# Optimization experiments

Hardware: AMD Instinct MI355X
Metric: run time of the kernel (lower is better)

The kernel has to match this reference:

```python
import jax, jax.numpy as jnp
import numpy as np

J = 4  # number of wavelet scales


def _wavelet(P, X, mask):
    """Graph diffusion wavelet features for one (batch, time) slice.
    P: [N,N] transition matrix, X: [N,F] node features, mask: [N].
    Returns flattened pooled features [K*F], K = 1 + J + J*(J-1)/2.
    """
    P_pow = P
    F1, F2, PSI = [], [], []
    for _ in range(J):
        new_P = P_pow @ P_pow              # P^{2^{i+1}}
        psi = new_P - P_pow                # psi_i = P^{2^{i+1}} - P^{2^i}
        sc = jnp.abs(psi @ X)              # |psi_i X|  [N,F]
        F1.append(sc)
        for prev_psi in PSI:               # second order: |psi_j |psi_i X||, j < i
            F2.append(jnp.abs(prev_psi @ sc))
        PSI.append(psi)
        P_pow = new_P
    F0 = P_pow @ X                         # zeroth order: P^{2^J} X
    feats = jnp.stack([F0, *F1, *F2])      # [K, N, F]
    # pooling: mean over nodes (normalized by mask.sum()), then flatten
    return (feats.sum(axis=1) / mask.sum()).reshape(-1)


def setup_inputs() -> dict:
    key = jax.random.key(0)
    k1, k2 = jax.random.split(key)
    B, T, N, F = 8, 4, 1024, 64
    A = jax.random.uniform(k1, (B, T, N, N), dtype=jnp.float32)
    P = A / A.sum(axis=-1, keepdims=True)  # row-stochastic transition matrix
    X = jax.random.normal(k2, (B, T, N, F), dtype=jnp.float32)
    mask = jnp.ones((B, T, N), dtype=jnp.float32)
    return {"P": P, "X": X, "mask": mask}


def reference(P, X, mask):
    return jax.vmap(jax.vmap(_wavelet))(P, X, mask)  # [B, T, K*F]
```

## Files before the change

kernel.cpp:

```cpp
#include <hip/hip_runtime.h>

typedef unsigned short u16;
typedef __bf16 bfx8 __attribute__((ext_vector_type(8)));
typedef float f32x4 __attribute__((ext_vector_type(4)));
typedef unsigned short u16x4 __attribute__((ext_vector_type(4)));

#define NN 1024
#define FF 64
#define NSLICE 32
#define KFEAT 11

#define POOL_BYTES (NSLICE * KFEAT * FF * 4)
#define MSUM_OFF   POOL_BYTES
#define SLICE0     ((size_t)1 << 20)
#define MB1        (1024u * 1024u)
#define KB128      (131072u)
#define KB256      (262144u)
#define OFF_P    0u
#define OFF_PT   (2u * MB1)
#define OFF_P2   (4u * MB1)
#define OFF_XT   (6u * MB1)
#define OFF_Y2T  (6u * MB1 + 1u * KB128)
#define OFF_Y4T  (6u * MB1 + 2u * KB128)
#define OFF_Y6T  (6u * MB1 + 3u * KB128)
#define OFF_Y8T  (6u * MB1 + 4u * KB128)
#define OFF_Y10T (6u * MB1 + 5u * KB128)
#define OFF_Y12T (6u * MB1 + 6u * KB128)
#define OFF_Y14T (6u * MB1 + 7u * KB128)
#define OFF_S1T  (6u * MB1 + 8u * KB128)
#define OFF_S2T  (6u * MB1 + 9u * KB128)
#define OFF_S3T  (6u * MB1 + 10u * KB128)
#define OFF_TQ2  (6u * MB1 + 11u * KB128)
#define OFF_TQ3  (6u * MB1 + 12u * KB128)
#define OFF_TW4  (6u * MB1 + 13u * KB128)
#define OFF_TP6  (6u * MB1 + 14u * KB128)
#define OFF_Y1   (8u * MB1)
#define OFF_Y2   (8u * MB1 + 1u * KB256)
#define OFF_Y4   (8u * MB1 + 2u * KB256)
#define OFF_Y8   (8u * MB1 + 3u * KB256)
#define OFF_PS1  (8u * MB1 + 4u * KB256)
#define OFF_PS2  (8u * MB1 + 5u * KB256)
#define OFF_PS3  (8u * MB1 + 6u * KB256)
#define OFF_QS2  (8u * MB1 + 7u * KB256)
#define OFF_QS3  (8u * MB1 + 8u * KB256)
#define OFF_W4   (8u * MB1 + 9u * KB256)
#define PS_BYTES ((size_t)(11u * MB1))

#define GL16(g, l) __builtin_amdgcn_global_load_lds( \
    (const __attribute__((address_space(1))) unsigned int*)(g), \
    (__attribute__((address_space(3))) unsigned int*)(l), 16, 0, 0)


__device__ __forceinline__ u16 f2b(float v) {
  __bf16 h = (__bf16)v;
  return __builtin_bit_cast(u16, h);
}

__global__ void k_convP(const float* __restrict__ P, char* ws, int sliceBase) {
  __shared__ float tile[64][65];
  int s = blockIdx.z;
  const float* Ps = P + (size_t)(sliceBase + s) * NN * NN;
  char* base = ws + SLICE0 + (size_t)s * PS_BYTES;
  u16* Pb  = (u16*)(base + OFF_P);
  u16* PbT = (u16*)(base + OFF_PT);
  int r0 = blockIdx.y * 64, c0 = blockIdx.x * 64;
  int tid = threadIdx.x;
  int tc = tid & 15, tr = tid >> 4;
  for (int rr = 0; rr < 64; rr += 16) {
    int r = rr + tr;
    float4 v = *(const float4*)&Ps[(size_t)(r0 + r) * NN + c0 + tc * 4];
    tile[r][tc * 4 + 0] = v.x;
    tile[r][tc * 4 + 1] = v.y;
    tile[r][tc * 4 + 2] = v.z;
    tile[r][tc * 4 + 3] = v.w;
    u16x4 pk = {f2b(v.x), f2b(v.y), f2b(v.z), f2b(v.w)};
    *(u16x4*)&Pb[(size_t)(r0 + r) * NN + c0 + tc * 4] = pk;
  }
  __syncthreads();
  for (int it = 0; it < 4; ++it) {
    int oc = (tid >> 4) + it * 16;
    int ch = tid & 15;
    u16x4 pk = {f2b(tile[ch * 4 + 0][oc]), f2b(tile[ch * 4 + 1][oc]),
                f2b(tile[ch * 4 + 2][oc]), f2b(tile[ch * 4 + 3][oc])};
    *(u16x4*)&PbT[(size_t)(c0 + oc) * NN + r0 + ch * 4] = pk;
  }
}

__global__ void k_convX(const float* __restrict__ X, char* ws, int sliceBase) {
  __shared__ float tile[64][65];
  int s = blockIdx.z;
  const float* Xs = X + (size_t)(sliceBase + s) * NN * FF;
  u16* XT = (u16*)(ws + SLICE0 + (size_t)s * PS_BYTES + OFF_XT);
  int r0 = blockIdx.x * 64;
  int tx = threadIdx.x & 63, ty = threadIdx.x >> 6;
  for (int rr = 0; rr < 64; rr += 4)
    tile[rr + ty][tx] = Xs[(size_t)(r0 + rr + ty) * FF + tx];
  __syncthreads();
  for (int rr = 0; rr < 64; rr += 4)
    XT[(size_t)(rr + ty) * NN + r0 + tx] = f2b(tile[tx][rr + ty]);
}

__global__ void k_msum(const float* __restrict__ mask, float* msum) {
  int s = blockIdx.x;
  const float* m = mask + (size_t)s * NN;
  int t = threadIdx.x;
  float v = m[t] + m[t + 256] + m[t + 512] + m[t + 768];
  for (int o = 32; o; o >>= 1) v += __shfl_down(v, o);
  __shared__ float ps[4];
  if ((t & 63) == 0) ps[t >> 6] = v;
  __syncthreads();
  if (t == 0) msum[s] = ps[0] + ps[1] + ps[2] + ps[3];
}

__global__ __launch_bounds__(256)
void k_square(char* ws) {
  __shared__ u16 sh[16384];

  unsigned nwg = gridDim.x, wg = blockIdx.x;
  unsigned newid = (wg & 7) * (nwg >> 3) + (wg >> 3);
  int z = newid >> 6;
  int by = (newid >> 3) & 7, bx = newid & 7;

  char* base = ws + SLICE0 + (size_t)z * PS_BYTES;
  const u16* A  = (const u16*)(base + OFF_P);
  const u16* Bt = (const u16*)(base + OFF_PT);
  u16* C        = (u16*)(base + OFF_P2);

  const int tid = threadIdx.x;
  const int lane = tid & 63, wave = tid >> 6;
  const int wr = wave >> 1, wc = wave & 1;
  const int l16 = lane & 15, lk = lane >> 4;
  const int bm = by * 128, bn = bx * 128;

  const int pc = (((tid & 3) - (tid >> 3)) & 3) << 3;
  const u16* gA = A + (size_t)(bm + (tid >> 2)) * NN + pc;
  const u16* gB = Bt + (size_t)(bn + (tid >> 2)) * NN + pc;
  const int rot = ((lk + (l16 >> 1)) & 3) << 3;

  f32x4 acc[4][4] = {};

#define SQ_STAGE(k0, buf)                                   \
  {                                                         \
    u16* dA = sh + (buf)*4096 + wave * 512;                 \
    u16* dB = sh + 8192 + (buf)*4096 + wave * 512;          \
    GL16(gA + (k0), dA);                                    \
    GL16(gA + 64 * NN + (k0), dA + 2048);                   \
    GL16(gB + (k0), dB);                                    \
    GL16(gB + 64 * NN + (k0), dB + 2048);                   \
  }

#define SQ_COMPUTE(buf)                                                      \
  {                                                                          \
    const u16* bA = sh + (buf)*4096;                                         \
    const u16* bB = sh + 8192 + (buf)*4096;                                  \
    bfx8 af[4], bf[4];                                                       \
    _Pragma("unroll") for (int m = 0; m < 4; ++m)                            \
        af[m] = *(const bfx8*)&bA[(wr * 64 + m * 16 + l16) * 32 + rot];      \
    _Pragma("unroll") for (int n = 0; n < 4; ++n)                            \
        bf[n] = *(const bfx8*)&bB[(wc * 64 + n * 16 + l16) * 32 + rot];      \
    __builtin_amdgcn_s_setprio(1);                                           \
    _Pragma("unroll") for (int m = 0; m < 4; ++m)                            \
        _Pragma("unroll") for (int n = 0; n < 4; ++n)                        \
            acc[m][n] = __builtin_amdgcn_mfma_f32_16x16x32_bf16(             \
                af[m], bf[n], acc[m][n], 0, 0, 0);                           \
    __builtin_amdgcn_s_setprio(0);                                           \
  }

  SQ_STAGE(0, 0);
#pragma unroll 2
  for (int t = 1; t < 32; ++t) {
    SQ_STAGE(t * 32, t & 1);
    asm volatile("s_waitcnt vmcnt(4)" ::: "memory");
    __builtin_amdgcn_s_barrier();
    SQ_COMPUTE((t - 1) & 1);
    __builtin_amdgcn_s_barrier();
  }
  asm volatile("s_waitcnt vmcnt(0)" ::: "memory");
  __builtin_amdgcn_s_barrier();
  SQ_COMPUTE(1);

#pragma unroll
  for (int m = 0; m < 4; ++m) {
    int row0 = bm + wr * 64 + m * 16 + lk * 4;
#pragma unroll
    for (int n = 0; n < 4; ++n) {
      int col = bn + wc * 64 + n * 16 + l16;
#pragma unroll
      for (int r = 0; r < 4; ++r)
        C[(size_t)(row0 + r) * NN + col] = f2b(acc[m][n][r]);
    }
  }
}

struct NA {
  int a, rawK;
  int bt[3], d[3], pk[3], f[3], ta[3], tv[3];
};

__device__ __forceinline__ void nar_epilogue(
    char* base, const f32x4 (&acc)[2][2], int bm, int wr, int wc, int l16,
    int lk, int lane, int dof, int pkI, int fo, int tao, int tvo, bool doRaw,
    int rawK, int poolBase, float* __restrict__ pooled) {
  const float* D = dof >= 0 ? (const float*)(base + dof) : nullptr;
  float* F  = fo  >= 0 ? (float*)(base + fo)  : nullptr;
  u16* Ta   = tao >= 0 ? (u16*)(base + tao)   : nullptr;
  u16* Tv   = tvo >= 0 ? (u16*)(base + tvo)   : nullptr;

  float ps[2] = {0.f, 0.f};
  float pr[2] = {0.f, 0.f};

#pragma unroll
  for (int m = 0; m < 2; ++m) {
    int row0 = bm + wr * 32 + m * 16 + lk * 4;
#pragma unroll
    for (int n = 0; n < 2; ++n) {
      int col = wc * 32 + n * 16 + l16;
      float v0 = acc[m][n][0], v1 = acc[m][n][1];
      float v2 = acc[m][n][2], v3 = acc[m][n][3];
      float w0 = v0, w1 = v1, w2 = v2, w3 = v3;
      if (D) {
        w0 = v0 - D[(size_t)(row0 + 0) * FF + col];
        w1 = v1 - D[(size_t)(row0 + 1) * FF + col];
        w2 = v2 - D[(size_t)(row0 + 2) * FF + col];
        w3 = v3 - D[(size_t)(row0 + 3) * FF + col];
      }
      float a0 = fabsf(w0), a1 = fabsf(w1), a2 = fabsf(w2), a3 = fabsf(w3);
      if (pkI >= 0) ps[n] += a0 + a1 + a2 + a3;
      if (doRaw) pr[n] += v0 + v1 + v2 + v3;
      if (F) {
        F[(size_t)(row0 + 0) * FF + col] = v0;
        F[(size_t)(row0 + 1) * FF + col] = v1;
        F[(size_t)(row0 + 2) * FF + col] = v2;
        F[(size_t)(row0 + 3) * FF + col] = v3;
      }
      if (Ta) {
        u16x4 pkk = {f2b(a0), f2b(a1), f2b(a2), f2b(a3)};
        *(u16x4*)&Ta[(size_t)col * NN + row0] = pkk;
      }
      if (Tv) {
        u16x4 pkk = {f2b(v0), f2b(v1), f2b(v2), f2b(v3)};
        *(u16x4*)&Tv[(size_t)col * NN + row0] = pkk;
      }
    }
  }

  if (pkI >= 0) {
#pragma unroll
    for (int n = 0; n < 2; ++n) {
      float v = ps[n];
      v += __shfl_xor(v, 16);
      v += __shfl_xor(v, 32);
      if (lane < 16)
        atomicAdd(&pooled[poolBase + pkI * FF + wc * 32 + n * 16 + lane], v);
    }
  }
  if (doRaw) {
#pragma unroll
    for (int n = 0; n < 2; ++n) {
      float v = pr[n];
      v += __shfl_xor(v, 16);
      v += __shfl_xor(v, 32);
      if (lane < 16)
        atomicAdd(&pooled[poolBase + rawK * FF + wc * 32 + n * 16 + lane], v);
    }
  }
}

template <int NB>
__global__ __launch_bounds__(256)
void k_nar(char* ws, int sliceBase, float* __restrict__ pooled, NA na) {
  __shared__ u16 sh[16384];
  unsigned nwg = gridDim.x, wg = blockIdx.x;
  unsigned newid = (wg & 7) * (nwg >> 3) + (wg >> 3);
  int by = newid & 15;
  int s = newid >> 4;
  char* base = ws + SLICE0 + (size_t)s * PS_BYTES;

  const u16* A = (const u16*)(base + na.a);
  int poolBase = (sliceBase + s) * (KFEAT * FF);

  const int tid = threadIdx.x;
  const int lane = tid & 63, wave = tid >> 6;
  const int wr = wave >> 1, wc = wave & 1;
  const int l16 = lane & 15, lk = lane >> 4;
  const int bm = by * 64;

  const int pc = (((tid & 3) - (tid >> 3)) & 3) << 3;
  const u16* gA = A + (size_t)(bm + (tid >> 2)) * NN + pc;
  const u16* gB[NB];
#pragma unroll
  for (int j = 0; j < NB; ++j)
    gB[j] = (const u16*)(base + na.bt[j]) + (size_t)(tid >> 2) * NN + pc;
  const int rot = ((lk + (l16 >> 1)) & 3) << 3;

  f32x4 acc[NB][2][2] = {};

  auto STAGE = [&](int k0, int buf) {
    u16* dA = sh + buf * 8192 + wave * 512;
    GL16(gA + k0, dA);
#pragma unroll
    for (int j = 0; j < NB; ++j) {
      u16* dB = sh + buf * 8192 + 2048 + j * 2048 + wave * 512;
      GL16(gB[j] + k0, dB);
    }
  };
  auto COMPUTE = [&](int buf) {
    const u16* bA = sh + buf * 8192;
    bfx8 af[2];
#pragma unroll
    for (int m = 0; m < 2; ++m)
      af[m] = *(const bfx8*)&bA[(wr * 32 + m * 16 + l16) * 32 + rot];
    __builtin_amdgcn_s_setprio(1);
#pragma unroll
    for (int j = 0; j < NB; ++j) {
      const u16* bB = sh + buf * 8192 + 2048 + j * 2048;
      bfx8 bf[2];
#pragma unroll
      for (int n = 0; n < 2; ++n)
        bf[n] = *(const bfx8*)&bB[(wc * 32 + n * 16 + l16) * 32 + rot];
#pragma unroll
      for (int m = 0; m < 2; ++m)
#pragma unroll
        for (int n = 0; n < 2; ++n)
          acc[j][m][n] = __builtin_amdgcn_mfma_f32_16x16x32_bf16(
              af[m], bf[n], acc[j][m][n], 0, 0, 0);
    }
    __builtin_amdgcn_s_setprio(0);
  };

  STAGE(0, 0);
#pragma unroll 2
  for (int t = 1; t < 32; ++t) {
    STAGE(t * 32, t & 1);
    if constexpr (NB == 2)
      asm volatile("s_waitcnt vmcnt(3)" ::: "memory");
    else
      asm volatile("s_waitcnt vmcnt(4)" ::: "memory");
    __builtin_amdgcn_s_barrier();
    COMPUTE((t - 1) & 1);
    __builtin_amdgcn_s_barrier();
  }
  asm volatile("s_waitcnt vmcnt(0)" ::: "memory");
  __builtin_amdgcn_s_barrier();
  COMPUTE(1);

#pragma unroll
  for (int j = 0; j < NB; ++j) {
    bool doRaw = (j == 0) && (na.rawK >= 0);
    nar_epilogue(base, acc[j], bm, wr, wc, l16, lk, lane, na.d[j], na.pk[j],
                 na.f[j], na.ta[j], na.tv[j], doRaw, na.rawK, poolBase, pooled);
  }
}

__global__ __launch_bounds__(256)
void k_nar64(char* ws, int sliceBase, float* __restrict__ pooled, NA na) {
  __shared__ u16 sh[16384];
  unsigned nwg = gridDim.x, wg = blockIdx.x;
  unsigned newid = (wg & 7) * (nwg >> 3) + (wg >> 3);
  int by = newid & 15;
  int s = newid >> 4;
  char* base = ws + SLICE0 + (size_t)s * PS_BYTES;

  const u16* A  = (const u16*)(base + na.a);
  const u16* Bt = (const u16*)(base + na.bt[0]);
  int poolBase = (sliceBase + s) * (KFEAT * FF);

  const int tid = threadIdx.x;
  const int lane = tid & 63, wave = tid >> 6;
  const int wr = wave >> 1, wc = wave & 1;
  const int l16 = lane & 15, lk = lane >> 4;
  const int bm = by * 64;

  const int srow = lane >> 3;
  const int lch = (((lane & 7) - (srow & 7)) & 7) * 8;
  const u16* gA0 = A + (size_t)(bm + wave * 16 + srow) * NN + lch;
  const u16* gA1 = A + (size_t)(bm + wave * 16 + 8 + srow) * NN + lch;
  const u16* gB0 = Bt + (size_t)(wave * 16 + srow) * NN + lch;
  const u16* gB1 = Bt + (size_t)(wave * 16 + 8 + srow) * NN + lch;

  const int r8 = l16 & 7;

  f32x4 acc[2][2] = {};

#define N64_STAGE(k0, buf)                                  \
  {                                                         \
    u16* dA = sh + (buf)*8192 + wave * 1024;                \
    u16* dB = sh + (buf)*8192 + 4096 + wave * 1024;         \
    GL16(gA0 + (k0), dA);                                   \
    GL16(gA1 + (k0), dA + 512);                             \
    GL16(gB0 + (k0), dB);                                   \
    GL16(gB1 + (k0), dB + 512);                             \
  }

#define N64_COMPUTE(buf)                                                     \
  {                                                                          \
    const u16* bA = sh + (buf)*8192;                                         \
    const u16* bB = sh + (buf)*8192 + 4096;                                  \
    _Pragma("unroll") for (int ks = 0; ks < 2; ++ks) {                       \
      const int ph = ((ks * 4 + lk + r8) & 7) * 8;                           \
      bfx8 af[2], bf[2];                                                     \
      _Pragma("unroll") for (int m = 0; m < 2; ++m)                          \
          af[m] = *(const bfx8*)&bA[(wr * 32 + m * 16 + l16) * 64 + ph];     \
      _Pragma("unroll") for (int n = 0; n < 2; ++n)                          \
          bf[n] = *(const bfx8*)&bB[(wc * 32 + n * 16 + l16) * 64 + ph];     \
      __builtin_amdgcn_s_setprio(1);                                        \
      _Pragma("unroll") for (int m = 0; m < 2; ++m)                          \
          _Pragma("unroll") for (int n = 0; n < 2; ++n)                      \
              acc[m][n] = __builtin_amdgcn_mfma_f32_16x16x32_bf16(           \
                  af[m], bf[n], acc[m][n], 0, 0, 0);                         \
      __builtin_amdgcn_s_setprio(0);                                        \
    }                                                                        \
  }

  N64_STAGE(0, 0);
#pragma unroll 2
  for (int t = 1; t < 16; ++t) {
    N64_STAGE(t * 64, t & 1);
    asm volatile("s_waitcnt vmcnt(4)" ::: "memory");
    __builtin_amdgcn_s_barrier();
    N64_COMPUTE((t - 1) & 1);
    __builtin_amdgcn_s_barrier();
  }
  asm volatile("s_waitcnt vmcnt(0)" ::: "memory");
  __builtin_amdgcn_s_barrier();
  N64_COMPUTE(1);

  bool doRaw = (na.rawK >= 0);
  nar_epilogue(base, acc, bm, wr, wc, l16, lk, lane, na.d[0], na.pk[0],
               na.f[0], na.ta[0], na.tv[0], doRaw, na.rawK, poolBase, pooled);
}

__global__ void k_final(const float* __restrict__ pooled, const float* __restrict__ msum,
                        float* __restrict__ out, int total) {
  int i = blockIdx.x * 256 + threadIdx.x;
  if (i < total) out[i] = pooled[i] / msum[i / (KFEAT * FF)];
}

static NA mk1(int a, int rawK, int bt, int d, int pk, int f, int ta, int tv) {
  NA x;
  x.a = a; x.rawK = rawK;
  for (int j = 0; j < 3; ++j) {
    x.bt[j] = -1; x.d[j] = -1; x.pk[j] = -1;
    x.f[j] = -1; x.ta[j] = -1; x.tv[j] = -1;
  }
  x.bt[0] = bt; x.d[0] = d; x.pk[0] = pk; x.f[0] = f; x.ta[0] = ta; x.tv[0] = tv;
  return x;
}
static void setslot(NA& x, int j, int bt, int d, int pk, int f, int ta, int tv) {
  x.bt[j] = bt; x.d[j] = d; x.pk[j] = pk; x.f[j] = f; x.ta[j] = ta; x.tv[j] = tv;
}

extern "C" void kernel_launch(void* const* d_in, const int* in_sizes, int n_in,
                              void* d_out, int out_size, void* d_ws, size_t ws_size,
                              hipStream_t stream) {
  const float* P = (const float*)d_in[0];
  const float* X = (const float*)d_in[1];
  const float* mask = (const float*)d_in[2];
  float* out = (float*)d_out;
  char* ws = (char*)d_ws;
  float* pooled = (float*)ws;
  float* msum = (float*)(ws + MSUM_OFF);

  hipMemsetAsync(pooled, 0, POOL_BYTES, stream);
  k_msum<<<NSLICE, 256, 0, stream>>>(mask, msum);

  int S = 1;
  if (ws_size > SLICE0 + PS_BYTES) S = (int)((ws_size - SLICE0) / PS_BYTES);
  if (S > NSLICE) S = NSLICE;
  if (S < 1) S = 1;

  for (int b0 = 0; b0 < NSLICE; b0 += S) {
    int n = (NSLICE - b0 < S) ? (NSLICE - b0) : S;
    k_convP<<<dim3(16, 16, n), 256, 0, stream>>>(P, ws, b0);
    k_convX<<<dim3(16, 1, n), 256, 0, stream>>>(X, ws, b0);
    k_square<<<64 * n, 256, 0, stream>>>(ws);

    NA c1 = mk1(OFF_P, -1, OFF_XT, -1, -1, OFF_Y1, -1, -1);
    k_nar64<<<16 * n, 256, 0, stream>>>(ws, b0, pooled, c1);
    NA c2 = mk1(OFF_P2, -1, OFF_XT, (int)OFF_Y1, 1, OFF_Y2, -1, OFF_Y2T);
    k_nar64<<<16 * n, 256, 0, stream>>>(ws, b0, pooled, c2);
    NA c3 = mk1(OFF_P2, -1, OFF_Y2T, (int)OFF_Y2, 2, OFF_Y4, OFF_S1T, OFF_Y4T);
    k_nar64<<<16 * n, 256, 0, stream>>>(ws, b0, pooled, c3);
    NA c4 = mk1(OFF_P2, -1, OFF_Y4T, -1, -1, -1, -1, OFF_Y6T);
    k_nar64<<<16 * n, 256, 0, stream>>>(ws, b0, pooled, c4);
    NA c5 = mk1(OFF_P2, -1, OFF_Y6T, (int)OFF_Y4, 3, OFF_Y8, OFF_S2T, OFF_Y8T);
    k_nar64<<<16 * n, 256, 0, stream>>>(ws, b0, pooled, c5);
    NA c6 = mk1(OFF_P2, -1, OFF_Y8T, -1, -1, -1, -1, OFF_Y10T);
    k_nar64<<<16 * n, 256, 0, stream>>>(ws, b0, pooled, c6);
    NA c7 = mk1(OFF_P2, -1, OFF_Y10T, -1, -1, -1, -1, OFF_Y12T);
    k_nar64<<<16 * n, 256, 0, stream>>>(ws, b0, pooled, c7);
    NA c8 = mk1(OFF_P2, -1, OFF_Y12T, -1, -1, -1, -1, OFF_Y14T);
    k_nar64<<<16 * n, 256, 0, stream>>>(ws, b0, pooled, c8);
    NA c9 = mk1(OFF_P2, 0, OFF_Y14T, (int)OFF_Y8, 4, -1, OFF_S3T, -1);
    k_nar64<<<16 * n, 256, 0, stream>>>(ws, b0, pooled, c9);

    NA c10 = mk1(OFF_P, -1, OFF_S1T, -1, -1, OFF_PS1, -1, -1);
    setslot(c10, 1, OFF_S2T, -1, -1, OFF_PS2, -1, -1);
    setslot(c10, 2, OFF_S3T, -1, -1, OFF_PS3, -1, -1);
    k_nar<3><<<16 * n, 256, 0, stream>>>(ws, b0, pooled, c10);
    NA c11 = mk1(OFF_P2, -1, OFF_S1T, (int)OFF_PS1, 5, -1, -1, -1);
    setslot(c11, 1, OFF_S2T, (int)OFF_PS2, 6, OFF_QS2, -1, OFF_TQ2);
    setslot(c11, 2, OFF_S3T, (int)OFF_PS3, 8, OFF_QS3, -1, OFF_TQ3);
    k_nar<3><<<16 * n, 256, 0, stream>>>(ws, b0, pooled, c11);
    NA c12 = mk1(OFF_P2, -1, OFF_TQ2, (int)OFF_QS2, 7, -1, -1, -1);
    setslot(c12, 1, OFF_TQ3, (int)OFF_QS3, 9, OFF_W4, -1, OFF_TW4);
    k_nar<2><<<16 * n, 256, 0, stream>>>(ws, b0, pooled, c12);
    NA c13 = mk1(OFF_P2, -1, OFF_TW4, -1, -1, -1, -1, OFF_TP6);
    k_nar64<<<16 * n, 256, 0, stream>>>(ws, b0, pooled, c13);
    NA c14 = mk1(OFF_P2, -1, OFF_TP6, (int)OFF_W4, 10, -1, -1, -1);
    k_nar64<<<16 * n, 256, 0, stream>>>(ws, b0, pooled, c14);
  }
  int total = NSLICE * KFEAT * FF;
  k_final<<<(total + 255) / 256, 256, 0, stream>>>(pooled, msum, out, total);
}
```

Measured before the change: 386.9 us.

## Fuse P and P2 GEMM pairs into shared-B dual-A kernels

Two new kernels compute P·B and P²·B in one pass over a shared B operand, fusing the c1/c2 and c10/c11 launches. They form the wavelet difference in registers instead of writing the intermediate Y1 and PS buffers and reading them back. This cuts two launches per batch of slices, halves the B-tile loads, and removes the round trips through those intermediates. It uses more LDS and accumulator registers per block, which can lower occupancy. The vmcnt wait inside k_nar for the NB==3 path changes from 4 to 2, but the only NB==3 launch (c10/c11) is removed, so that edit affects no running code path.

```diff
diff --git a/kernel.cpp b/kernel.cpp
--- a/kernel.cpp
+++ b/kernel.cpp
@@ -34,16 +34,12 @@
 #define OFF_TQ3  (6u * MB1 + 12u * KB128)
 #define OFF_TW4  (6u * MB1 + 13u * KB128)
 #define OFF_TP6  (6u * MB1 + 14u * KB128)
-#define OFF_Y1   (8u * MB1)
-#define OFF_Y2   (8u * MB1 + 1u * KB256)
-#define OFF_Y4   (8u * MB1 + 2u * KB256)
-#define OFF_Y8   (8u * MB1 + 3u * KB256)
-#define OFF_PS1  (8u * MB1 + 4u * KB256)
-#define OFF_PS2  (8u * MB1 + 5u * KB256)
-#define OFF_PS3  (8u * MB1 + 6u * KB256)
-#define OFF_QS2  (8u * MB1 + 7u * KB256)
-#define OFF_QS3  (8u * MB1 + 8u * KB256)
-#define OFF_W4   (8u * MB1 + 9u * KB256)
+#define OFF_Y2   (8u * MB1)
+#define OFF_Y4   (8u * MB1 + 1u * KB256)
+#define OFF_Y8   (8u * MB1 + 2u * KB256)
+#define OFF_QS2  (8u * MB1 + 3u * KB256)
+#define OFF_QS3  (8u * MB1 + 4u * KB256)
+#define OFF_W4   (8u * MB1 + 5u * KB256)
 #define PS_BYTES ((size_t)(11u * MB1))
 
 #define GL16(g, l) __builtin_amdgcn_global_load_lds( \
@@ -335,7 +331,7 @@
     if constexpr (NB == 2)
       asm volatile("s_waitcnt vmcnt(3)" ::: "memory");
     else
-      asm volatile("s_waitcnt vmcnt(4)" ::: "memory");
+      asm volatile("s_waitcnt vmcnt(2)" ::: "memory");
     __builtin_amdgcn_s_barrier();
     COMPUTE((t - 1) & 1);
     __builtin_amdgcn_s_barrier();
@@ -430,6 +426,225 @@
                na.f[0], na.ta[0], na.tv[0], doRaw, na.rawK, poolBase, pooled);
 }
 
+__global__ __launch_bounds__(256)
+void k_nC12(char* ws, int sliceBase, float* __restrict__ pooled) {
+  __shared__ u16 sh[12288];
+  unsigned nwg = gridDim.x, wg = blockIdx.x;
+  unsigned newid = (wg & 7) * (nwg >> 3) + (wg >> 3);
+  int by = newid & 15;
+  int s = newid >> 4;
+  char* base = ws + SLICE0 + (size_t)s * PS_BYTES;
+
+  const u16* A0 = (const u16*)(base + OFF_P);
+  const u16* A1 = (const u16*)(base + OFF_P2);
+  const u16* Bt = (const u16*)(base + OFF_XT);
+  float* Y2 = (float*)(base + OFF_Y2);
+  u16* Y2T = (u16*)(base + OFF_Y2T);
+  int poolBase = (sliceBase + s) * (KFEAT * FF);
+
+  const int tid = threadIdx.x;
+  const int lane = tid & 63, wave = tid >> 6;
+  const int wr = wave >> 1, wc = wave & 1;
+  const int l16 = lane & 15, lk = lane >> 4;
+  const int bm = by * 64;
+
+  const int pc = (((tid & 3) - (tid >> 3)) & 3) << 3;
+  const u16* gA0 = A0 + (size_t)(bm + (tid >> 2)) * NN + pc;
+  const u16* gA1 = A1 + (size_t)(bm + (tid >> 2)) * NN + pc;
+  const u16* gB  = Bt + (size_t)(tid >> 2) * NN + pc;
+  const int rot = ((lk + (l16 >> 1)) & 3) << 3;
+
+  f32x4 acc[2][2][2] = {};
+
+  auto STAGE = [&](int k0, int buf) {
+    GL16(gA0 + k0, sh + buf * 6144 + wave * 512);
+    GL16(gA1 + k0, sh + buf * 6144 + 2048 + wave * 512);
+    GL16(gB + k0, sh + buf * 6144 + 4096 + wave * 512);
+  };
+  auto COMPUTE = [&](int buf) {
+    const u16* bA0 = sh + buf * 6144;
+    const u16* bA1 = sh + buf * 6144 + 2048;
+    const u16* bB  = sh + buf * 6144 + 4096;
+    bfx8 a0[2], a1[2], bf[2];
+#pragma unroll
+    for (int m = 0; m < 2; ++m) {
+      a0[m] = *(const bfx8*)&bA0[(wr * 32 + m * 16 + l16) * 32 + rot];
+      a1[m] = *(const bfx8*)&bA1[(wr * 32 + m * 16 + l16) * 32 + rot];
+    }
+#pragma unroll
+    for (int n = 0; n < 2; ++n)
+      bf[n] = *(const bfx8*)&bB[(wc * 32 + n * 16 + l16) * 32 + rot];
+    __builtin_amdgcn_s_setprio(1);
+#pragma unroll
+    for (int m = 0; m < 2; ++m)
+#pragma unroll
+      for (int n = 0; n < 2; ++n) {
+        acc[0][m][n] = __builtin_amdgcn_mfma_f32_16x16x32_bf16(a0[m], bf[n], acc[0][m][n], 0, 0, 0);
+        acc[1][m][n] = __builtin_amdgcn_mfma_f32_16x16x32_bf16(a1[m], bf[n], acc[1][m][n], 0, 0, 0);
+      }
+    __builtin_amdgcn_s_setprio(0);
+  };
+
+  STAGE(0, 0);
+#pragma unroll 2
+  for (int t = 1; t < 32; ++t) {
+    STAGE(t * 32, t & 1);
+    asm volatile("s_waitcnt vmcnt(3)" ::: "memory");
+    __builtin_amdgcn_s_barrier();
+    COMPUTE((t - 1) & 1);
+    __builtin_amdgcn_s_barrier();
+  }
+  asm volatile("s_waitcnt vmcnt(0)" ::: "memory");
+  __builtin_amdgcn_s_barrier();
+  COMPUTE(1);
+
+  float ps[2] = {0.f, 0.f};
+#pragma unroll
+  for (int m = 0; m < 2; ++m) {
+    int row0 = bm + wr * 32 + m * 16 + lk * 4;
+#pragma unroll
+    for (int n = 0; n < 2; ++n) {
+      int col = wc * 32 + n * 16 + l16;
+#pragma unroll
+      for (int r = 0; r < 4; ++r) {
+        float v = acc[1][m][n][r];
+        float w = v - acc[0][m][n][r];
+        ps[n] += fabsf(w);
+        Y2[(size_t)(row0 + r) * FF + col] = v;
+      }
+      u16x4 pkk = {f2b(acc[1][m][n][0]), f2b(acc[1][m][n][1]),
+                   f2b(acc[1][m][n][2]), f2b(acc[1][m][n][3])};
+      *(u16x4*)&Y2T[(size_t)col * NN + row0] = pkk;
+    }
+  }
+#pragma unroll
+  for (int n = 0; n < 2; ++n) {
+    float v = ps[n];
+    v += __shfl_xor(v, 16);
+    v += __shfl_xor(v, 32);
+    if (lane < 16)
+      atomicAdd(&pooled[poolBase + 1 * FF + wc * 32 + n * 16 + lane], v);
+  }
+}
+
+__global__ __launch_bounds__(256)
+void k_nC1011(char* ws, int sliceBase, float* __restrict__ pooled) {
+  __shared__ u16 sh[20480];
+  unsigned nwg = gridDim.x, wg = blockIdx.x;
+  unsigned newid = (wg & 7) * (nwg >> 3) + (wg >> 3);
+  int by = newid & 15;
+  int s = newid >> 4;
+  char* base = ws + SLICE0 + (size_t)s * PS_BYTES;
+
+  const u16* A0 = (const u16*)(base + OFF_P);
+  const u16* A1 = (const u16*)(base + OFF_P2);
+  int poolBase = (sliceBase + s) * (KFEAT * FF);
+
+  const int tid = threadIdx.x;
+  const int lane = tid & 63, wave = tid >> 6;
+  const int wr = wave >> 1, wc = wave & 1;
+  const int l16 = lane & 15, lk = lane >> 4;
+  const int bm = by * 64;
+
+  const int pc = (((tid & 3) - (tid >> 3)) & 3) << 3;
+  const u16* gA0 = A0 + (size_t)(bm + (tid >> 2)) * NN + pc;
+  const u16* gA1 = A1 + (size_t)(bm + (tid >> 2)) * NN + pc;
+  const unsigned btOff[3] = {OFF_S1T, OFF_S2T, OFF_S3T};
+  const u16* gB[3];
+#pragma unroll
+  for (int j = 0; j < 3; ++j)
+    gB[j] = (const u16*)(base + btOff[j]) + (size_t)(tid >> 2) * NN + pc;
+  const int rot = ((lk + (l16 >> 1)) & 3) << 3;
+
+  f32x4 acc[2][3][2][2] = {};
+
+  auto STAGE = [&](int k0, int buf) {
+    GL16(gA0 + k0, sh + buf * 10240 + wave * 512);
+    GL16(gA1 + k0, sh + buf * 10240 + 2048 + wave * 512);
+#pragma unroll
+    for (int j = 0; j < 3; ++j)
+      GL16(gB[j] + k0, sh + buf * 10240 + 4096 + j * 2048 + wave * 512);
+  };
+  auto COMPUTE = [&](int buf) {
+    const u16* bA0 = sh + buf * 10240;
+    const u16* bA1 = sh + buf * 10240 + 2048;
+    bfx8 a0[2], a1[2];
+#pragma unroll
+    for (int m = 0; m < 2; ++m) {
+      a0[m] = *(const bfx8*)&bA0[(wr * 32 + m * 16 + l16) * 32 + rot];
+      a1[m] = *(const bfx8*)&bA1[(wr * 32 + m * 16 + l16) * 32 + rot];
+    }
+    __builtin_amdgcn_s_setprio(1);
+#pragma unroll
+    for (int j = 0; j < 3; ++j) {
+      const u16* bB = sh + buf * 10240 + 4096 + j * 2048;
+      bfx8 bf[2];
+#pragma unroll
+      for (int n = 0; n < 2; ++n)
+        bf[n] = *(const bfx8*)&bB[(wc * 32 + n * 16 + l16) * 32 + rot];
+#pragma unroll
+      for (int m = 0; m < 2; ++m)
+#pragma unroll
+        for (int n = 0; n < 2; ++n) {
+          acc[0][j][m][n] = __builtin_amdgcn_mfma_f32_16x16x32_bf16(a0[m], bf[n], acc[0][j][m][n], 0, 0, 0);
+          acc[1][j][m][n] = __builtin_amdgcn_mfma_f32_16x16x32_bf16(a1[m], bf[n], acc[1][j][m][n], 0, 0, 0);
+        }
+    }
+    __builtin_amdgcn_s_setprio(0);
+  };
+
+  STAGE(0, 0);
+#pragma unroll 2
+  for (int t = 1; t < 32; ++t) {
+    STAGE(t * 32, t & 1);
+    asm volatile("s_waitcnt vmcnt(5)" ::: "memory");
+    __builtin_amdgcn_s_barrier();
+    COMPUTE((t - 1) & 1);
+    __builtin_amdgcn_s_barrier();
+  }
+  asm volatile("s_waitcnt vmcnt(0)" ::: "memory");
+  __builtin_amdgcn_s_barrier();
+  COMPUTE(1);
+
+  const int pks[3] = {5, 6, 8};
+#pragma unroll
+  for (int j = 0; j < 3; ++j) {
+    float* F = j == 1 ? (float*)(base + OFF_QS2)
+                      : (j == 2 ? (float*)(base + OFF_QS3) : nullptr);
+    u16* Tv = j == 1 ? (u16*)(base + OFF_TQ2)
+                     : (j == 2 ? (u16*)(base + OFF_TQ3) : nullptr);
+    float ps[2] = {0.f, 0.f};
+#pragma unroll
+    for (int m = 0; m < 2; ++m) {
+      int row0 = bm + wr * 32 + m * 16 + lk * 4;
+#pragma unroll
+      for (int n = 0; n < 2; ++n) {
+        int col = wc * 32 + n * 16 + l16;
+#pragma unroll
+        for (int r = 0; r < 4; ++r) {
+          float v = acc[1][j][m][n][r];
+          float w = v - acc[0][j][m][n][r];
+          ps[n] += fabsf(w);
+          if (F) F[(size_t)(row0 + r) * FF + col] = v;
+        }
+        if (Tv) {
+          u16x4 pkk = {f2b(acc[1][j][m][n][0]), f2b(acc[1][j][m][n][1]),
+                       f2b(acc[1][j][m][n][2]), f2b(acc[1][j][m][n][3])};
+          *(u16x4*)&Tv[(size_t)col * NN + row0] = pkk;
+        }
+      }
+    }
+#pragma unroll
+    for (int n = 0; n < 2; ++n) {
+      float v = ps[n];
+      v += __shfl_xor(v, 16);
+      v += __shfl_xor(v, 32);
+      if (lane < 16)
+        atomicAdd(&pooled[poolBase + pks[j] * FF + wc * 32 + n * 16 + lane], v);
+    }
+  }
+}
+
 __global__ void k_final(const float* __restrict__ pooled, const float* __restrict__ msum,
                         float* __restrict__ out, int total) {
   int i = blockIdx.x * 256 + threadIdx.x;
@@ -475,10 +690,7 @@
     k_convX<<<dim3(16, 1, n), 256, 0, stream>>>(X, ws, b0);
     k_square<<<64 * n, 256, 0, stream>>>(ws);
 
-    NA c1 = mk1(OFF_P, -1, OFF_XT, -1, -1, OFF_Y1, -1, -1);
-    k_nar64<<<16 * n, 256, 0, stream>>>(ws, b0, pooled, c1);
-    NA c2 = mk1(OFF_P2, -1, OFF_XT, (int)OFF_Y1, 1, OFF_Y2, -1, OFF_Y2T);
-    k_nar64<<<16 * n, 256, 0, stream>>>(ws, b0, pooled, c2);
+    k_nC12<<<16 * n, 256, 0, stream>>>(ws, b0, pooled);
     NA c3 = mk1(OFF_P2, -1, OFF_Y2T, (int)OFF_Y2, 2, OFF_Y4, OFF_S1T, OFF_Y4T);
     k_nar64<<<16 * n, 256, 0, stream>>>(ws, b0, pooled, c3);
     NA c4 = mk1(OFF_P2, -1, OFF_Y4T, -1, -1, -1, -1, OFF_Y6T);
@@ -494,14 +706,7 @@
     NA c9 = mk1(OFF_P2, 0, OFF_Y14T, (int)OFF_Y8, 4, -1, OFF_S3T, -1);
     k_nar64<<<16 * n, 256, 0, stream>>>(ws, b0, pooled, c9);
 
-    NA c10 = mk1(OFF_P, -1, OFF_S1T, -1, -1, OFF_PS1, -1, -1);
-    setslot(c10, 1, OFF_S2T, -1, -1, OFF_PS2, -1, -1);
-    setslot(c10, 2, OFF_S3T, -1, -1, OFF_PS3, -1, -1);
-    k_nar<3><<<16 * n, 256, 0, stream>>>(ws, b0, pooled, c10);
-    NA c11 = mk1(OFF_P2, -1, OFF_S1T, (int)OFF_PS1, 5, -1, -1, -1);
-    setslot(c11, 1, OFF_S2T, (int)OFF_PS2, 6, OFF_QS2, -1, OFF_TQ2);
-    setslot(c11, 2, OFF_S3T, (int)OFF_PS3, 8, OFF_QS3, -1, OFF_TQ3);
-    k_nar<3><<<16 * n, 256, 0, stream>>>(ws, b0, pooled, c11);
+    k_nC1011<<<16 * n, 256, 0, stream>>>(ws, b0, pooled);
     NA c12 = mk1(OFF_P2, -1, OFF_TQ2, (int)OFF_QS2, 7, -1, -1, -1);
     setslot(c12, 1, OFF_TQ3, (int)OFF_QS3, 9, OFF_W4, -1, OFF_TW4);
     k_nar<2><<<16 * n, 256, 0, stream>>>(ws, b0, pooled, c12);
```

Result: faster. 358.0 us (median of 2 runs) (-7.5%).
